# Kernel tuning notes

Hardware: AMD Instinct MI355X
Metric: run time of the kernel (lower is better)

The kernel has to match this reference:

```python
import jax, jax.numpy as jnp
import numpy as np

B, T, C, H = 2, 2048, 1024, 16
HD = C // H            # 64
LAYER_IDX, N_LAYER = 5, 12
BASE = 16
# window_mode='power_2.0': progress=(5+1)/12=0.5; window=max(16, int(16+0.5**2*(2048-16)))=524
WINDOW = max(BASE, int(BASE + ((LAYER_IDX + 1) / N_LAYER) ** 2.0 * (T - BASE)))
WINDOW = min(WINDOW, T)


def setup_inputs() -> dict:
    key = jax.random.key(0)
    ks = jax.random.split(key, 6)
    x = jax.random.normal(ks[0], (B, T, C), dtype=jnp.float32)
    Wq = jax.random.normal(ks[1], (C, C), dtype=jnp.float32) * 0.02
    Wk = jax.random.normal(ks[2], (C, C), dtype=jnp.float32) * 0.02
    Wv = jax.random.normal(ks[3], (C, C), dtype=jnp.float32) * 0.02
    Wo = jax.random.normal(ks[4], (C, C), dtype=jnp.float32) * 0.02
    # RoPE tables: angles theta_i = t / 10000^(i/(HD/2)), shape (T,1,HD//2) to broadcast over (B,T,H,HD//2)
    half = HD // 2
    inv_freq = 1.0 / (10000.0 ** (jnp.arange(half, dtype=jnp.float32) / half))
    ang = jnp.arange(T, dtype=jnp.float32)[:, None] * inv_freq[None, :]  # (T, half)
    rope_cos = jnp.cos(ang)[:, None, :]  # (T,1,half)
    rope_sin = jnp.sin(ang)[:, None, :]
    return {"x": x, "Wq": Wq, "Wk": Wk, "Wv": Wv, "Wo": Wo,
            "rope_cos": rope_cos, "rope_sin": rope_sin}


def _apply_rotary(x, cos, sin):
    d = x.shape[-1] // 2
    x1, x2 = x[..., :d], x[..., d:]
    return jnp.concatenate([x1 * cos + x2 * sin, -x2 * sin + x1 * cos], axis=-1)


def reference(x, Wq, Wk, Wv, Wo, rope_cos, rope_sin):
    Bv, Tv, Cv = x.shape
    q = (x @ Wq).reshape(Bv, Tv, H, HD)
    k = (x @ Wk).reshape(Bv, Tv, H, HD)
    v = (x @ Wv).reshape(Bv, Tv, H, HD)
    q = _apply_rotary(q, rope_cos, rope_sin)
    k = _apply_rotary(k, rope_cos, rope_sin)
    # sliding-window causal mask: cols<=rows and cols>=rows-WINDOW+1
    rows = jnp.arange(Tv)[:, None]
    cols = jnp.arange(Tv)[None, :]
    allowed = (cols <= rows) & (cols >= rows - WINDOW + 1)  # (T,T)
    scale = 1.0 / np.sqrt(HD)
    scores = jnp.einsum('bthd,bshd->bhts', q, k) * scale  # (B,H,T,T)
    scores = jnp.where(allowed[None, None], scores, -jnp.inf)
    attn = jax.nn.softmax(scores, axis=-1)
    y = jnp.einsum('bhts,bshd->bthd', attn, v).reshape(Bv, Tv, Cv)
    return y @ Wo
```

## Files before the change

### kernel.cpp

```cpp
#include <hip/hip_runtime.h>
#include <math.h>

typedef unsigned short u16;
typedef unsigned int u32;
typedef __bf16 bf16x8 __attribute__((ext_vector_type(8)));
typedef float f32x4 __attribute__((ext_vector_type(4)));
typedef unsigned short ushort4v __attribute__((ext_vector_type(4)));

#define T_SEQ 2048
#define WIN_M1 523
#define QSCALE 0.180336879f
#define MASKV -1e30f
#define MINIT -3000.0f

__device__ __forceinline__ u16 f2b(float f) {
  union { float f; unsigned int u; } v; v.f = f;
  unsigned int u = v.u;
  u += 0x7FFFu + ((u >> 16) & 1u);
  return (u16)(u >> 16);
}

__device__ __forceinline__ u32 cvtpk(float lo, float hi) {
  u32 r;
  asm("v_cvt_pk_bf16_f32 %0, %1, %2" : "=v"(r) : "v"(lo), "v"(hi));
  return r;
}

__device__ __forceinline__ void load_lds16(const u16* g, u16* l) {
  __builtin_amdgcn_global_load_lds(
      (const __attribute__((address_space(1))) void*)g,
      (__attribute__((address_space(3))) void*)l, 16, 0, 0);
}

__global__ void convert_x_k(const float* __restrict__ x, u16* __restrict__ xb) {
  int i = blockIdx.x * blockDim.x + threadIdx.x;
  float4 v = ((const float4*)x)[i];
  u16* d = xb + i * 4;
  d[0] = f2b(v.x); d[1] = f2b(v.y); d[2] = f2b(v.z); d[3] = f2b(v.w);
}

__global__ void transpose_w4_k(const float* __restrict__ W0, const float* __restrict__ W1,
                               const float* __restrict__ W2, const float* __restrict__ W3,
                               u16* __restrict__ WcatT, u16* __restrict__ WoT) {
  __shared__ float tile[32][33];
  const int z = blockIdx.z;
  const float* W = (z == 0) ? W0 : (z == 1) ? W1 : (z == 2) ? W2 : W3;
  u16* Wt = (z < 3) ? (WcatT + (size_t)z * 1024 * 1024) : WoT;
  int tx = threadIdx.x & 31, ty = threadIdx.x >> 5;
  int n0 = blockIdx.x * 32, k0 = blockIdx.y * 32;
#pragma unroll
  for (int i = 0; i < 4; ++i)
    tile[ty + i * 8][tx] = W[(size_t)(k0 + ty + i * 8) * 1024 + n0 + tx];
  __syncthreads();
#pragma unroll
  for (int i = 0; i < 4; ++i)
    Wt[(size_t)(n0 + ty + i * 8) * 1024 + k0 + tx] = f2b(tile[tx][ty + i * 8]);
}

template <int MODE>
__global__ __launch_bounds__(256) void gemm_k(
    const u16* __restrict__ A, const u16* __restrict__ Bt,
    float* __restrict__ outf,
    u16* __restrict__ Qo, u16* __restrict__ Ko, u16* __restrict__ Vto,
    const float* __restrict__ rc, const float* __restrict__ rs) {
  __shared__ alignas(16) u16 As[2][128 * 32];
  __shared__ alignas(16) u16 Bs[2][128 * 32];
  const int tid = threadIdx.x, lane = tid & 63, w = tid >> 6;
  const int l15 = lane & 15, q4 = lane >> 4;
  const int row0 = blockIdx.y * 128, col0 = blockIdx.x * 128;
  const int wm = w >> 1, wn = w & 1;

  f32x4 acc[4][4];
#pragma unroll
  for (int i = 0; i < 4; ++i)
#pragma unroll
    for (int j = 0; j < 4; ++j) acc[i][j] = (f32x4){0.f, 0.f, 0.f, 0.f};

  const int off0 = (w * 2) * 1024 + lane * 16;
  const int r0 = off0 >> 6, c0 = (off0 & 63) >> 1;
  const int off1 = off0 + 1024;
  const int r1 = off1 >> 6, c1 = (off1 & 63) >> 1;
  const u16* gA0 = A + (size_t)(row0 + r0) * 1024 + c0;
  const u16* gA1 = A + (size_t)(row0 + r1) * 1024 + c1;
  const u16* gB0 = Bt + (size_t)(col0 + r0) * 1024 + c0;
  const u16* gB1 = Bt + (size_t)(col0 + r1) * 1024 + c1;
  const int soff = (w * 2) * 512;

  auto stage = [&](int buf, int k0) {
    load_lds16(gA0 + k0, &As[buf][soff]);
    load_lds16(gA1 + k0, &As[buf][soff + 512]);
    load_lds16(gB0 + k0, &Bs[buf][soff]);
    load_lds16(gB1 + k0, &Bs[buf][soff + 512]);
  };
  auto compute = [&](int buf) {
    bf16x8 af[4], bfr[4];
#pragma unroll
    for (int im = 0; im < 4; ++im)
      af[im] = *(const bf16x8*)&As[buf][(wm * 64 + im * 16 + l15) * 32 + q4 * 8];
#pragma unroll
    for (int jn = 0; jn < 4; ++jn)
      bfr[jn] = *(const bf16x8*)&Bs[buf][(wn * 64 + jn * 16 + l15) * 32 + q4 * 8];
#pragma unroll
    for (int im = 0; im < 4; ++im)
#pragma unroll
      for (int jn = 0; jn < 4; ++jn)
        acc[im][jn] = __builtin_amdgcn_mfma_f32_16x16x32_bf16(af[im], bfr[jn], acc[im][jn], 0, 0, 0);
  };

  stage(0, 0);
  __syncthreads();
  int cur = 0;
  for (int k0 = 32; k0 < 1024; k0 += 32) {
    stage(cur ^ 1, k0);
    compute(cur);
    __syncthreads();
    cur ^= 1;
  }
  compute(cur);

  if constexpr (MODE == 0) {
#pragma unroll
    for (int im = 0; im < 4; ++im) {
      const int rowb = row0 + wm * 64 + im * 16 + q4 * 4;
      const int b = rowb >> 11, t0 = rowb & 2047;
#pragma unroll
      for (int jn = 0; jn < 2; ++jn) {
        const int n = col0 + wn * 64 + jn * 16 + l15;
        const int sel = n >> 10, nn = n & 1023;
        const int h = nn >> 6, hd = nn & 63;
        if (sel < 2) {
          const float qs = (sel == 0) ? QSCALE : 1.0f;
          u16* dst = (sel == 0 ? Qo : Ko) + ((size_t)(b * 16 + h) * 2048) * 64;
#pragma unroll
          for (int r = 0; r < 4; ++r) {
            const int t = t0 + r;
            const float c = rc[t * 32 + hd], s = rs[t * 32 + hd];
            const float x1 = acc[im][jn][r], x2 = acc[im][jn + 2][r];
            dst[(size_t)t * 64 + hd] = f2b((x1 * c + x2 * s) * qs);
            dst[(size_t)t * 64 + hd + 32] = f2b((x1 * c - x2 * s) * qs);
          }
        } else {
          ushort4v p1, p2;
#pragma unroll
          for (int r = 0; r < 4; ++r) {
            p1[r] = f2b(acc[im][jn][r]);
            p2[r] = f2b(acc[im][jn + 2][r]);
          }
          u16* dst = Vto + (size_t)(b * 16 + h) * 64 * 2048 + t0;
          *(ushort4v*)(dst + (size_t)hd * 2048) = p1;
          *(ushort4v*)(dst + (size_t)(hd + 32) * 2048) = p2;
        }
      }
    }
  } else {
#pragma unroll
    for (int im = 0; im < 4; ++im) {
      const int rowb = row0 + wm * 64 + im * 16 + q4 * 4;
#pragma unroll
      for (int jn = 0; jn < 4; ++jn) {
        const int n = col0 + wn * 64 + jn * 16 + l15;
#pragma unroll
        for (int r = 0; r < 4; ++r)
          outf[(size_t)(rowb + r) * 1024 + n] = acc[im][jn][r];
      }
    }
  }
}

__global__ __launch_bounds__(256) void attn_k(
    const u16* __restrict__ Q, const u16* __restrict__ Kk,
    const u16* __restrict__ Vt, u16* __restrict__ Y) {
  const int lane = threadIdx.x & 63, w = threadIdx.x >> 6;
  const int l15 = lane & 15, q4 = lane >> 4;
  const int qt = blockIdx.x & 15, bh = blockIdx.x >> 4;
  const int q0 = qt * 128 + w * 32;
  const u16* Qb = Q + (size_t)bh * 2048 * 64;
  const u16* Kb = Kk + (size_t)bh * 2048 * 64;
  const u16* Vb = Vt + (size_t)bh * 64 * 2048;

  bf16x8 bq[2][2];
#pragma unroll
  for (int qs = 0; qs < 2; ++qs)
#pragma unroll
    for (int kb = 0; kb < 2; ++kb)
      bq[qs][kb] = *(const bf16x8*)(Qb + (size_t)(q0 + qs * 16 + l15) * 64 + kb * 32 + q4 * 8);

  f32x4 o[2][4];
#pragma unroll
  for (int qs = 0; qs < 2; ++qs)
#pragma unroll
    for (int jo = 0; jo < 4; ++jo) o[qs][jo] = (f32x4){0.f, 0.f, 0.f, 0.f};
  float m[2] = {MINIT, MINIT}, lsum[2] = {0.f, 0.f};

  int s0 = q0 - WIN_M1; if (s0 < 0) s0 = 0; s0 &= ~31;
  const int srcA = l15 + ((q4 & 1) << 5);
  const int srcB = srcA + 16;
  const bool lowq4 = (q4 < 2);

  bf16x8 kc[2][2], kn[2][2];
#pragma unroll
  for (int ks = 0; ks < 2; ++ks)
#pragma unroll
    for (int kb = 0; kb < 2; ++kb)
      kc[ks][kb] = *(const bf16x8*)(Kb + (size_t)(s0 + ks * 16 + l15) * 64 + kb * 32 + q4 * 8);

  int kv0 = s0;

#define TILE_BODY(KC, KN)                                                              \
  {                                                                                    \
    bf16x8 vr[4];                                                                      \
    _Pragma("unroll") for (int jo = 0; jo < 4; ++jo)                                   \
        vr[jo] = *(const bf16x8*)(Vb + (size_t)(jo * 16 + l15) * 2048 + kv0 + q4 * 8); \
    f32x4 ss[2][2];                                                                    \
    _Pragma("unroll") for (int ks = 0; ks < 2; ++ks)                                   \
        _Pragma("unroll") for (int qs = 0; qs < 2; ++qs)                               \
            ss[ks][qs] = (f32x4){0.f, 0.f, 0.f, 0.f};                                  \
    _Pragma("unroll") for (int kb = 0; kb < 2; ++kb)                                   \
        _Pragma("unroll") for (int ks = 0; ks < 2; ++ks)                               \
            _Pragma("unroll") for (int qs = 0; qs < 2; ++qs)                           \
                ss[ks][qs] = __builtin_amdgcn_mfma_f32_16x16x32_bf16(                  \
                    KC[ks][kb], bq[qs][kb], ss[ks][qs], 0, 0, 0);                      \
    const int kvn = kv0 + 32;                                                          \
    if (kvn <= q0) {                                                                   \
      _Pragma("unroll") for (int ks = 0; ks < 2; ++ks)                                 \
          _Pragma("unroll") for (int kb = 0; kb < 2; ++kb)                             \
              KN[ks][kb] = *(const bf16x8*)(Kb + (size_t)(kvn + ks * 16 + l15) * 64 +  \
                                            kb * 32 + q4 * 8);                         \
    }                                                                                  \
    if ((kv0 + 32 > q0) || (kv0 < q0 - 492)) {                                         \
      _Pragma("unroll") for (int qs = 0; qs < 2; ++qs) {                               \
        const int tq = q0 + qs * 16 + l15;                                             \
        _Pragma("unroll") for (int ks = 0; ks < 2; ++ks)                               \
            _Pragma("unroll") for (int r = 0; r < 4; ++r) {                            \
          const int kv = kv0 + ks * 16 + q4 * 4 + r;                                   \
          if (kv > tq || kv < tq - WIN_M1) ss[ks][qs][r] = MASKV;                      \
        }                                                                              \
      }                                                                                \
    }                                                                                  \
    float tmax[2];                                                                     \
    _Pragma("unroll") for (int qs = 0; qs < 2; ++qs) {                                 \
      float a = fmaxf(fmaxf(ss[0][qs][0], ss[0][qs][1]),                               \
                      fmaxf(ss[0][qs][2], ss[0][qs][3]));                              \
      float b = fmaxf(fmaxf(ss[1][qs][0], ss[1][qs][1]),                               \
                      fmaxf(ss[1][qs][2], ss[1][qs][3]));                              \
      float tm = fmaxf(a, b);                                                          \
      tm = fmaxf(tm, __shfl_xor(tm, 16));                                              \
      tm = fmaxf(tm, __shfl_xor(tm, 32));                                              \
      tmax[qs] = tm;                                                                   \
    }                                                                                  \
    const int pred = (tmax[0] <= m[0] + 8.f) && (tmax[1] <= m[1] + 8.f);               \
    if (!__all(pred)) {                                                                \
      _Pragma("unroll") for (int qs = 0; qs < 2; ++qs) {                               \
        const float mn = fmaxf(m[qs], tmax[qs]);                                       \
        const float sc = exp2f(m[qs] - mn);                                            \
        m[qs] = mn; lsum[qs] *= sc;                                                    \
        _Pragma("unroll") for (int r = 0; r < 4; ++r) {                                \
          const float sr = __shfl(sc, q4 * 4 + r);                                     \
          _Pragma("unroll") for (int jo = 0; jo < 4; ++jo) o[qs][jo][r] *= sr;         \
        }                                                                              \
      }                                                                                \
    }                                                                                  \
    _Pragma("unroll") for (int qs = 0; qs < 2; ++qs) {                                 \
      const float mm = m[qs];                                                          \
      float p[2][4];                                                                   \
      _Pragma("unroll") for (int ks = 0; ks < 2; ++ks)                                 \
          _Pragma("unroll") for (int r = 0; r < 4; ++r)                                \
              p[ks][r] = exp2f(ss[ks][qs][r] - mm);                                    \
      float rsv = ((p[0][0] + p[0][1]) + (p[0][2] + p[0][3])) +                        \
                  ((p[1][0] + p[1][1]) + (p[1][2] + p[1][3]));                         \
      rsv += __shfl_xor(rsv, 16);                                                      \
      rsv += __shfl_xor(rsv, 32);                                                      \
      lsum[qs] += rsv;                                                                 \
      const u32 a0 = cvtpk(p[0][0], p[0][1]), a1 = cvtpk(p[0][2], p[0][3]);            \
      const u32 b0 = cvtpk(p[1][0], p[1][1]), b1 = cvtpk(p[1][2], p[1][3]);            \
      union { u32 d[4]; bf16x8 v; } pu;                                                \
      const u32 d0a = (u32)__shfl((int)a0, srcA), d0b = (u32)__shfl((int)b0, srcA);    \
      const u32 d1a = (u32)__shfl((int)a1, srcA), d1b = (u32)__shfl((int)b1, srcA);    \
      const u32 d2a = (u32)__shfl((int)a0, srcB), d2b = (u32)__shfl((int)b0, srcB);    \
      const u32 d3a = (u32)__shfl((int)a1, srcB), d3b = (u32)__shfl((int)b1, srcB);    \
      pu.d[0] = lowq4 ? d0a : d0b;                                                     \
      pu.d[1] = lowq4 ? d1a : d1b;                                                     \
      pu.d[2] = lowq4 ? d2a : d2b;                                                     \
      pu.d[3] = lowq4 ? d3a : d3b;                                                     \
      _Pragma("unroll") for (int jo = 0; jo < 4; ++jo)                                 \
          o[qs][jo] = __builtin_amdgcn_mfma_f32_16x16x32_bf16(pu.v, vr[jo],            \
                                                              o[qs][jo], 0, 0, 0);     \
    }                                                                                  \
  }

  while (true) {
    TILE_BODY(kc, kn);
    kv0 += 32; if (kv0 > q0) break;
    TILE_BODY(kn, kc);
    kv0 += 32; if (kv0 > q0) break;
  }
#undef TILE_BODY

  const int b = bh >> 4, h = bh & 15;
  u16* Yb = Y + (size_t)(b * 2048 + q0) * 1024 + h * 64 + l15;
#pragma unroll
  for (int qs = 0; qs < 2; ++qs)
#pragma unroll
    for (int r = 0; r < 4; ++r) {
      const float lv = __shfl(lsum[qs], q4 * 4 + r);
      const float inv = 1.0f / lv;
      u16* yr = Yb + (size_t)(qs * 16 + q4 * 4 + r) * 1024;
#pragma unroll
      for (int jo = 0; jo < 4; ++jo) yr[jo * 16] = f2b(o[qs][jo][r] * inv);
    }
}

extern "C" void kernel_launch(void* const* d_in, const int* in_sizes, int n_in,
                              void* d_out, int out_size, void* d_ws, size_t ws_size,
                              hipStream_t stream) {
  const float* x = (const float*)d_in[0];
  const float* Wq = (const float*)d_in[1];
  const float* Wk = (const float*)d_in[2];
  const float* Wv = (const float*)d_in[3];
  const float* Wo = (const float*)d_in[4];
  const float* rc = (const float*)d_in[5];
  const float* rs = (const float*)d_in[6];
  float* out = (float*)d_out;
  char* ws = (char*)d_ws;
  const size_t MB = 1024 * 1024;
  u16* xb = (u16*)(ws);
  u16* WcatT = (u16*)(ws + 8 * MB);
  u16* WoT = (u16*)(ws + 14 * MB);
  u16* Qr = (u16*)(ws + 16 * MB);
  u16* Kr = (u16*)(ws + 24 * MB);
  u16* Vt = (u16*)(ws + 32 * MB);
  u16* Y = (u16*)(ws + 40 * MB);

  convert_x_k<<<4096, 256, 0, stream>>>(x, xb);
  transpose_w4_k<<<dim3(32, 32, 4), 256, 0, stream>>>(Wq, Wk, Wv, Wo, WcatT, WoT);
  gemm_k<0><<<dim3(24, 32), 256, 0, stream>>>(xb, WcatT, nullptr, Qr, Kr, Vt, rc, rs);
  attn_k<<<512, 256, 0, stream>>>(Qr, Kr, Vt, Y);
  gemm_k<1><<<dim3(8, 32), 256, 0, stream>>>(Y, WoT, out, nullptr, nullptr, nullptr, nullptr, nullptr);
}
```

Baseline: 118.0 us.

## Deepen GEMM LDS pipeline to four stages and XOR-swizzle LDS layout

The projection GEMM now keeps four LDS buffers instead of two and prefetches two k-tiles ahead. It replaces __syncthreads with explicit vmcnt waits plus s_barrier, so global-to-LDS loads overlap compute across more iterations. It also applies an XOR swizzle to the 16-byte chunk column in both the global-load addressing and the fragment reads, to reduce LDS bank conflicts. Doubling LDS use (64KB per block) may lower occupancy. With a 4-buffer ring and only one barrier per iteration, the correctness of buffer reuse depends on the wait counts.

```diff
diff --git a/kernel.cpp b/kernel.cpp
--- a/kernel.cpp
+++ b/kernel.cpp
@@ -63,12 +63,13 @@
     float* __restrict__ outf,
     u16* __restrict__ Qo, u16* __restrict__ Ko, u16* __restrict__ Vto,
     const float* __restrict__ rc, const float* __restrict__ rs) {
-  __shared__ alignas(16) u16 As[2][128 * 32];
-  __shared__ alignas(16) u16 Bs[2][128 * 32];
+  __shared__ alignas(16) u16 As[4][128 * 32];
+  __shared__ alignas(16) u16 Bs[4][128 * 32];
   const int tid = threadIdx.x, lane = tid & 63, w = tid >> 6;
   const int l15 = lane & 15, q4 = lane >> 4;
   const int row0 = blockIdx.y * 128, col0 = blockIdx.x * 128;
   const int wm = w >> 1, wn = w & 1;
+  constexpr int NT = 32;
 
   f32x4 acc[4][4];
 #pragma unroll
@@ -76,30 +77,32 @@
 #pragma unroll
     for (int j = 0; j < 4; ++j) acc[i][j] = (f32x4){0.f, 0.f, 0.f, 0.f};
 
-  const int off0 = (w * 2) * 1024 + lane * 16;
-  const int r0 = off0 >> 6, c0 = (off0 & 63) >> 1;
-  const int off1 = off0 + 1024;
-  const int r1 = off1 >> 6, c1 = (off1 & 63) >> 1;
-  const u16* gA0 = A + (size_t)(row0 + r0) * 1024 + c0;
-  const u16* gA1 = A + (size_t)(row0 + r1) * 1024 + c1;
-  const u16* gB0 = Bt + (size_t)(col0 + r0) * 1024 + c0;
-  const u16* gB1 = Bt + (size_t)(col0 + r1) * 1024 + c1;
-  const int soff = (w * 2) * 512;
-
-  auto stage = [&](int buf, int k0) {
+  const int gsw = (lane & 3) ^ ((lane >> 2) & 3) ^ ((lane >> 4) & 3);
+  const int r0 = w * 32 + (lane >> 2);
+  const int r1 = r0 + 16;
+  const u16* gA0 = A + (size_t)(row0 + r0) * 1024 + gsw * 8;
+  const u16* gA1 = A + (size_t)(row0 + r1) * 1024 + gsw * 8;
+  const u16* gB0 = Bt + (size_t)(col0 + r0) * 1024 + gsw * 8;
+  const u16* gB1 = Bt + (size_t)(col0 + r1) * 1024 + gsw * 8;
+  const int soff = w * 1024;
+
+  auto stage = [&](int buf, int t) {
+    const int k0 = t * 32;
     load_lds16(gA0 + k0, &As[buf][soff]);
     load_lds16(gA1 + k0, &As[buf][soff + 512]);
     load_lds16(gB0 + k0, &Bs[buf][soff]);
     load_lds16(gB1 + k0, &Bs[buf][soff + 512]);
   };
+
+  const int gq = q4 ^ (l15 & 3) ^ ((l15 >> 2) & 3);
   auto compute = [&](int buf) {
     bf16x8 af[4], bfr[4];
 #pragma unroll
     for (int im = 0; im < 4; ++im)
-      af[im] = *(const bf16x8*)&As[buf][(wm * 64 + im * 16 + l15) * 32 + q4 * 8];
+      af[im] = *(const bf16x8*)&As[buf][(wm * 64 + im * 16 + l15) * 32 + gq * 8];
 #pragma unroll
     for (int jn = 0; jn < 4; ++jn)
-      bfr[jn] = *(const bf16x8*)&Bs[buf][(wn * 64 + jn * 16 + l15) * 32 + q4 * 8];
+      bfr[jn] = *(const bf16x8*)&Bs[buf][(wn * 64 + jn * 16 + l15) * 32 + gq * 8];
 #pragma unroll
     for (int im = 0; im < 4; ++im)
 #pragma unroll
@@ -108,15 +111,21 @@
   };
 
   stage(0, 0);
-  __syncthreads();
-  int cur = 0;
-  for (int k0 = 32; k0 < 1024; k0 += 32) {
-    stage(cur ^ 1, k0);
-    compute(cur);
-    __syncthreads();
-    cur ^= 1;
+  stage(1, 1);
+  int t = 0;
+  for (; t + 2 < NT; ++t) {
+    stage((t + 2) & 3, t + 2);
+    asm volatile("s_waitcnt vmcnt(8)" ::: "memory");
+    __builtin_amdgcn_s_barrier();
+    compute(t & 3);
   }
-  compute(cur);
+  asm volatile("s_waitcnt vmcnt(4)" ::: "memory");
+  __builtin_amdgcn_s_barrier();
+  compute(t & 3);
+  ++t;
+  asm volatile("s_waitcnt vmcnt(0)" ::: "memory");
+  __builtin_amdgcn_s_barrier();
+  compute(t & 3);
 
   if constexpr (MODE == 0) {
 #pragma unroll
@@ -133,11 +142,11 @@
           u16* dst = (sel == 0 ? Qo : Ko) + ((size_t)(b * 16 + h) * 2048) * 64;
 #pragma unroll
           for (int r = 0; r < 4; ++r) {
-            const int t = t0 + r;
-            const float c = rc[t * 32 + hd], s = rs[t * 32 + hd];
+            const int tt = t0 + r;
+            const float c = rc[tt * 32 + hd], s = rs[tt * 32 + hd];
             const float x1 = acc[im][jn][r], x2 = acc[im][jn + 2][r];
-            dst[(size_t)t * 64 + hd] = f2b((x1 * c + x2 * s) * qs);
-            dst[(size_t)t * 64 + hd + 32] = f2b((x1 * c - x2 * s) * qs);
+            dst[(size_t)tt * 64 + hd] = f2b((x1 * c + x2 * s) * qs);
+            dst[(size_t)tt * 64 + hd + 32] = f2b((x1 * c - x2 * s) * qs);
           }
         } else {
           ushort4v p1, p2;
```

New measurement: 119.1 us. No clear change (+1.0%).

## Prefetch next K/V tiles in attention and tighten GEMM pipeline sync

Applied to the files above, without the earlier changes.

The attention loop now loads the next tile's K and V fragments into registers at the top of each iteration, before the QK MFMAs, where before V was loaded only for the current tile. The GEMM main loop replaces __syncthreads with an explicit s_waitcnt vmcnt(4) plus raw s_barrier, so the next stage's async loads can stay in flight while the current stage is computed. The GEMM launch bounds also add a minimum of 4 blocks per SM. Together these aim to hide global-load latency, at the cost of more registers for the double-buffered V and possible spills under the occupancy hint.

```diff
diff --git a/kernel.cpp b/kernel.cpp
--- a/kernel.cpp
+++ b/kernel.cpp
@@ -58,7 +58,7 @@
 }
 
 template <int MODE>
-__global__ __launch_bounds__(256) void gemm_k(
+__global__ __launch_bounds__(256, 4) void gemm_k(
     const u16* __restrict__ A, const u16* __restrict__ Bt,
     float* __restrict__ outf,
     u16* __restrict__ Qo, u16* __restrict__ Ko, u16* __restrict__ Vto,
@@ -69,6 +69,7 @@
   const int l15 = lane & 15, q4 = lane >> 4;
   const int row0 = blockIdx.y * 128, col0 = blockIdx.x * 128;
   const int wm = w >> 1, wn = w & 1;
+  constexpr int NT = 32;
 
   f32x4 acc[4][4];
 #pragma unroll
@@ -86,7 +87,8 @@
   const u16* gB1 = Bt + (size_t)(col0 + r1) * 1024 + c1;
   const int soff = (w * 2) * 512;
 
-  auto stage = [&](int buf, int k0) {
+  auto stage = [&](int buf, int t) {
+    const int k0 = t * 32;
     load_lds16(gA0 + k0, &As[buf][soff]);
     load_lds16(gA1 + k0, &As[buf][soff + 512]);
     load_lds16(gB0 + k0, &Bs[buf][soff]);
@@ -108,15 +110,16 @@
   };
 
   stage(0, 0);
-  __syncthreads();
-  int cur = 0;
-  for (int k0 = 32; k0 < 1024; k0 += 32) {
-    stage(cur ^ 1, k0);
-    compute(cur);
-    __syncthreads();
-    cur ^= 1;
+  for (int t = 0; t + 1 < NT; ++t) {
+    stage((t + 1) & 1, t + 1);
+    asm volatile("s_waitcnt vmcnt(4)" ::: "memory");
+    __builtin_amdgcn_s_barrier();
+    compute(t & 1);
+    __builtin_amdgcn_s_barrier();
   }
-  compute(cur);
+  asm volatile("s_waitcnt vmcnt(0)" ::: "memory");
+  __builtin_amdgcn_s_barrier();
+  compute((NT - 1) & 1);
 
   if constexpr (MODE == 0) {
 #pragma unroll
@@ -133,11 +136,11 @@
           u16* dst = (sel == 0 ? Qo : Ko) + ((size_t)(b * 16 + h) * 2048) * 64;
 #pragma unroll
           for (int r = 0; r < 4; ++r) {
-            const int t = t0 + r;
-            const float c = rc[t * 32 + hd], s = rs[t * 32 + hd];
+            const int tt = t0 + r;
+            const float c = rc[tt * 32 + hd], s = rs[tt * 32 + hd];
             const float x1 = acc[im][jn][r], x2 = acc[im][jn + 2][r];
-            dst[(size_t)t * 64 + hd] = f2b((x1 * c + x2 * s) * qs);
-            dst[(size_t)t * 64 + hd + 32] = f2b((x1 * c - x2 * s) * qs);
+            dst[(size_t)tt * 64 + hd] = f2b((x1 * c + x2 * s) * qs);
+            dst[(size_t)tt * 64 + hd + 32] = f2b((x1 * c - x2 * s) * qs);
           }
         } else {
           ushort4v p1, p2;
@@ -198,19 +201,30 @@
   const bool lowq4 = (q4 < 2);
 
   bf16x8 kc[2][2], kn[2][2];
+  bf16x8 vc[4], vn[4];
 #pragma unroll
   for (int ks = 0; ks < 2; ++ks)
 #pragma unroll
     for (int kb = 0; kb < 2; ++kb)
       kc[ks][kb] = *(const bf16x8*)(Kb + (size_t)(s0 + ks * 16 + l15) * 64 + kb * 32 + q4 * 8);
+#pragma unroll
+  for (int jo = 0; jo < 4; ++jo)
+    vc[jo] = *(const bf16x8*)(Vb + (size_t)(jo * 16 + l15) * 2048 + s0 + q4 * 8);
 
   int kv0 = s0;
 
-#define TILE_BODY(KC, KN)                                                              \
+#define TILE_BODY(KC, VC, KN, VN)                                                      \
   {                                                                                    \
-    bf16x8 vr[4];                                                                      \
-    _Pragma("unroll") for (int jo = 0; jo < 4; ++jo)                                   \
-        vr[jo] = *(const bf16x8*)(Vb + (size_t)(jo * 16 + l15) * 2048 + kv0 + q4 * 8); \
+    const int kvn = kv0 + 32;                                                          \
+    if (kvn <= q0) {                                                                   \
+      _Pragma("unroll") for (int ks = 0; ks < 2; ++ks)                                 \
+          _Pragma("unroll") for (int kb = 0; kb < 2; ++kb)                             \
+              KN[ks][kb] = *(const bf16x8*)(Kb + (size_t)(kvn + ks * 16 + l15) * 64 +  \
+                                            kb * 32 + q4 * 8);                         \
+      _Pragma("unroll") for (int jo = 0; jo < 4; ++jo)                                 \
+          VN[jo] = *(const bf16x8*)(Vb + (size_t)(jo * 16 + l15) * 2048 + kvn +        \
+                                    q4 * 8);                                           \
+    }                                                                                  \
     f32x4 ss[2][2];                                                                    \
     _Pragma("unroll") for (int ks = 0; ks < 2; ++ks)                                   \
         _Pragma("unroll") for (int qs = 0; qs < 2; ++qs)                               \
@@ -220,13 +234,6 @@
             _Pragma("unroll") for (int qs = 0; qs < 2; ++qs)                           \
                 ss[ks][qs] = __builtin_amdgcn_mfma_f32_16x16x32_bf16(                  \
                     KC[ks][kb], bq[qs][kb], ss[ks][qs], 0, 0, 0);                      \
-    const int kvn = kv0 + 32;                                                          \
-    if (kvn <= q0) {                                                                   \
-      _Pragma("unroll") for (int ks = 0; ks < 2; ++ks)                                 \
-          _Pragma("unroll") for (int kb = 0; kb < 2; ++kb)                             \
-              KN[ks][kb] = *(const bf16x8*)(Kb + (size_t)(kvn + ks * 16 + l15) * 64 +  \
-                                            kb * 32 + q4 * 8);                         \
-    }                                                                                  \
     if ((kv0 + 32 > q0) || (kv0 < q0 - 492)) {                                         \
       _Pragma("unroll") for (int qs = 0; qs < 2; ++qs) {                               \
         const int tq = q0 + qs * 16 + l15;                                             \
@@ -283,15 +290,15 @@
       pu.d[2] = lowq4 ? d2a : d2b;                                                     \
       pu.d[3] = lowq4 ? d3a : d3b;                                                     \
       _Pragma("unroll") for (int jo = 0; jo < 4; ++jo)                                 \
-          o[qs][jo] = __builtin_amdgcn_mfma_f32_16x16x32_bf16(pu.v, vr[jo],            \
+          o[qs][jo] = __builtin_amdgcn_mfma_f32_16x16x32_bf16(pu.v, VC[jo],            \
                                                               o[qs][jo], 0, 0, 0);     \
     }                                                                                  \
   }
 
   while (true) {
-    TILE_BODY(kc, kn);
+    TILE_BODY(kc, vc, kn, vn);
     kv0 += 32; if (kv0 > q0) break;
-    TILE_BODY(kn, kc);
+    TILE_BODY(kn, vn, kc, vc);
     kv0 += 32; if (kv0 > q0) break;
   }
 #undef TILE_BODY
```

Result: faster. 112.4 us (-4.7%).
